# Optimization experiments

Measured on AMD Instinct MI355X. Metric: run time of the kernel, lower is better.

Reference implementation:

```python
import jax, jax.numpy as jnp
import numpy as np

B, T, S, D = 32, 1024, 1024, 512
VOCAB = 1000
INSERT_TOK = jnp.array([1, 2], dtype=jnp.int64)


def setup_inputs() -> dict:
    key = jax.random.key(0)
    k1, k2, k3, k4, k5 = jax.random.split(key, 5)
    input_var = jax.random.randint(k1, (B, T), 0, VOCAB, dtype=jnp.int64)
    output = jax.random.normal(k2, (B, T, D), jnp.float32)
    context = jax.random.normal(k3, (B, S, D), jnp.float32)
    # nn.Linear(2*dim, dim): weight [D, 2D], bias [D]
    W = jax.random.normal(k4, (D, 2 * D), jnp.float32) / np.sqrt(2 * D)
    b = jax.random.normal(k5, (D,), jnp.float32) * 0.01
    return {"input_var": input_var, "output": output, "context": context,
            "di": 0, "W": W, "b": b}


def _hard_align(input_var, src_len):
    """Replicates the python double-loop: sequential 'inserted' counter per batch.
    Returns (j, valid): j[b,i] = column of the 1.0 in attn row i (torch negative
    indices wrapped), valid[b,i] = whether row i gets any 1.0 at all."""
    bsz, tgt_len = input_var.shape
    flags = jnp.isin(input_var, INSERT_TOK)  # [B,T] is token an insert token

    def step(inserted, xi):
        i, flag = xi  # i: scalar position, flag: [B]
        cond = (src_len >= i - inserted)                    # gate, per batch
        ins2 = inserted + jnp.where(cond & flag, 1, 0)      # increment before write
        j = i - ins2 - 1
        j = jnp.where(j < 0, j + src_len, j)                # torch negative-index wrap
        return ins2, (j, cond)

    idxs = jnp.arange(1, tgt_len, dtype=jnp.int32)
    init = jnp.zeros((bsz,), jnp.int32)  # init_inserted()
    _, (j_rows, valid) = jax.lax.scan(step, init, (idxs, flags[:, 1:].T))
    j_rows = j_rows.T      # [B,T-1]
    valid = valid.T        # [B,T-1]
    # row 0: attn[b,0,0] = 1.0 always
    j_full = jnp.concatenate([jnp.zeros((bsz, 1), j_rows.dtype), j_rows], axis=1)
    valid_full = jnp.concatenate([jnp.ones((bsz, 1), bool), valid], axis=1)
    return j_full, valid_full


def reference(input_var, output, context, di, W, b):
    bsz, tgt_len, hid = output.shape
    src_len = context.shape[1]
    j, valid = _hard_align(input_var, src_len)              # [B,T], [B,T]
    vf = valid[:, :, None].astype(output.dtype)
    # hard one-hot attention matrix (as the module materializes it)
    attn = jax.nn.one_hot(j, src_len, dtype=output.dtype) * vf  # [B,T,S]
    # mix = bmm(attn, context) == masked gather of context rows
    mix = jnp.take_along_axis(context, j[:, :, None].astype(jnp.int32), axis=1) * vf
    combined = jnp.concatenate([mix, output], axis=-1)      # [B,T,2D]
    out = jnp.tanh(combined @ W.T + b)                      # [B,T,D]
    return out, attn
```

## Files before the change

### kernel.cpp

```cpp
#include <hip/hip_runtime.h>
#include <hip/hip_bf16.h>

#define B_ 32
#define T_ 1024
#define S_ 1024
#define D_ 512
#define M_ (B_*T_)
#define N_ D_
#define K_ (2*D_)

typedef __attribute__((ext_vector_type(8))) short bf16x8;
typedef __attribute__((ext_vector_type(4))) float f32x4;

__device__ inline unsigned short f2bf(float x) {
    union { float f; unsigned u; } v; v.f = x;
    unsigned r = v.u + 0x7FFFu + ((v.u >> 16) & 1u);
    return (unsigned short)(r >> 16);
}

__device__ inline float fast_tanh(float x) {
#if __has_builtin(__builtin_amdgcn_exp2f) && __has_builtin(__builtin_amdgcn_rcpf)
    const float e = __builtin_amdgcn_exp2f(x * 2.885390082f);
    const float r = __builtin_amdgcn_rcpf(e + 1.0f);
    return 1.0f - 2.0f * r;
#else
    return tanhf(x);
#endif
}

__global__ void align_kernel(const int* __restrict__ iv, int* __restrict__ jbuf) {
    const int b = blockIdx.x;
    const int lane = threadIdx.x;
    const int* row = iv + b * T_;
    int f[16];
    int local = 0;
    const int t0 = lane * 16;
    #pragma unroll
    for (int q = 0; q < 16; ++q) {
        const int t = t0 + q;
        const int tok = row[t];
        const int fl = (t > 0 && (tok == 1 || tok == 2)) ? 1 : 0;
        f[q] = fl;
        local += fl;
    }
    int incl = local;
    #pragma unroll
    for (int off = 1; off < 64; off <<= 1) {
        const int up = __shfl_up(incl, off, 64);
        if (lane >= off) incl += up;
    }
    int run = incl - local;
    #pragma unroll
    for (int q = 0; q < 16; ++q) {
        const int t = t0 + q;
        run += f[q];
        int j;
        if (t == 0) {
            j = 0;
        } else {
            j = t - run - 1;
            if (j < 0) j += S_;
        }
        jbuf[b * T_ + t] = j;
    }
}

__global__ void pack_w(const float* __restrict__ W, unsigned short* __restrict__ Wbf) {
    const int idx = blockIdx.x * blockDim.x + threadIdx.x;
    const f32x4 a = ((const f32x4*)W)[idx * 2];
    const f32x4 c = ((const f32x4*)W)[idx * 2 + 1];
    union { bf16x8 v; unsigned short u[8]; } pk;
    pk.u[0] = f2bf(a[0]); pk.u[1] = f2bf(a[1]); pk.u[2] = f2bf(a[2]); pk.u[3] = f2bf(a[3]);
    pk.u[4] = f2bf(c[0]); pk.u[5] = f2bf(c[1]); pk.u[6] = f2bf(c[2]); pk.u[7] = f2bf(c[3]);
    *(bf16x8*)(Wbf + (size_t)idx * 8) = pk.v;
}

__global__ __launch_bounds__(256)
void pack_a_attn(const float* __restrict__ ctx, const float* __restrict__ outp,
                 const int* __restrict__ jbuf, unsigned short* __restrict__ Abf,
                 float* __restrict__ attn) {
    const int m0 = blockIdx.x * 2;
    const int tid = threadIdx.x;
    const int r  = tid >> 7;
    const int kc = tid & 127;
    const int m  = m0 + r;
    const int k0 = kc * 8;
    const int j0 = jbuf[m0];
    const int j1 = jbuf[m0 + 1];

    const int jm = r ? j1 : j0;
    const float* src;
    if (k0 < D_) {
        const int b = m >> 10;
        src = ctx + ((size_t)(b * S_ + jm)) * D_ + k0;
    } else {
        src = outp + (size_t)m * D_ + (k0 - D_);
    }
    const f32x4 a = ((const f32x4*)src)[0];
    const f32x4 c = ((const f32x4*)src)[1];
    union { bf16x8 v; unsigned short u[8]; } pk;
    pk.u[0] = f2bf(a[0]); pk.u[1] = f2bf(a[1]); pk.u[2] = f2bf(a[2]); pk.u[3] = f2bf(a[3]);
    pk.u[4] = f2bf(c[0]); pk.u[5] = f2bf(c[1]); pk.u[6] = f2bf(c[2]); pk.u[7] = f2bf(c[3]);
    *(bf16x8*)(Abf + (size_t)m * K_ + k0) = pk.v;

    f32x4 v0 = {0.f, 0.f, 0.f, 0.f};
    f32x4 v1 = {0.f, 0.f, 0.f, 0.f};
    if ((j0 >> 2) == tid) v0[j0 & 3] = 1.0f;
    if ((j1 >> 2) == tid) v1[j1 & 3] = 1.0f;
    ((f32x4*)(attn + (size_t)m0 * S_))[tid] = v0;
    ((f32x4*)(attn + (size_t)(m0 + 1) * S_))[tid] = v1;
}

#define BM 128
#define BN 128
#define BK 64

template <bool PACKED>
__global__ __launch_bounds__(256)
void gemm_bt_tanh(const unsigned short* __restrict__ Abf,
                  const unsigned short* __restrict__ Wbf,
                  const float* __restrict__ bias,
                  float* __restrict__ out,
                  const float* __restrict__ ctx,
                  const float* __restrict__ outp,
                  const int* __restrict__ jbuf) {
    __shared__ unsigned short As[BM * BK];
    __shared__ unsigned short Bs[BN * BK];

    const int tid  = threadIdx.x;
    const int lane = tid & 63;
    const int wave = tid >> 6;
    const int wm = wave >> 1, wn = wave & 1;
    const int l16 = lane & 15, quad = lane >> 4;

    const int bm = blockIdx.x & 255;
    const int bn = blockIdx.x >> 8;
    const int mBase = bm * BM;
    const int nBase = bn * BN;

    f32x4 acc[4][4] = {};

    for (int ko = 0; ko < K_; ko += BK) {
        #pragma unroll
        for (int it = 0; it < 4; ++it) {
            const int chunk = it * 256 + tid;
            const int row = chunk >> 3;
            const int kc  = chunk & 7;
            const int gk8 = (kc ^ (row & 7)) * 8;
            if (PACKED) {
                const unsigned short* gA = Abf + (size_t)(mBase + row) * K_ + ko + gk8;
                __builtin_amdgcn_global_load_lds(
                    (const __attribute__((address_space(1))) void*)gA,
                    (__attribute__((address_space(3))) void*)(As + chunk * 8), 16, 0, 0);
            } else {
                const int kg = ko + gk8;
                const int m = mBase + row;
                const float* src;
                if (kg < D_) {
                    const int b = m >> 10;
                    src = ctx + ((size_t)(b * S_ + jbuf[m])) * D_ + kg;
                } else {
                    src = outp + (size_t)m * D_ + (kg - D_);
                }
                const f32x4 a = ((const f32x4*)src)[0];
                const f32x4 c = ((const f32x4*)src)[1];
                union { bf16x8 v; unsigned short u[8]; } pk;
                pk.u[0]=f2bf(a[0]); pk.u[1]=f2bf(a[1]); pk.u[2]=f2bf(a[2]); pk.u[3]=f2bf(a[3]);
                pk.u[4]=f2bf(c[0]); pk.u[5]=f2bf(c[1]); pk.u[6]=f2bf(c[2]); pk.u[7]=f2bf(c[3]);
                *(bf16x8*)(As + chunk * 8) = pk.v;
            }
        }
        #pragma unroll
        for (int it = 0; it < 4; ++it) {
            const int chunk = it * 256 + tid;
            const int row = chunk >> 3;
            const int kc  = chunk & 7;
            const int gk8 = (kc ^ (row & 7)) * 8;
            const unsigned short* gB = Wbf + (size_t)(nBase + row) * K_ + ko + gk8;
            __builtin_amdgcn_global_load_lds(
                (const __attribute__((address_space(1))) void*)gB,
                (__attribute__((address_space(3))) void*)(Bs + chunk * 8), 16, 0, 0);
        }
        __syncthreads();

        #pragma unroll
        for (int ks = 0; ks < 2; ++ks) {
            bf16x8 af[4], bfr[4];
            #pragma unroll
            for (int mt = 0; mt < 4; ++mt) {
                const int r = wm * 64 + mt * 16 + l16;
                const int q = ks * 4 + quad;
                af[mt] = *(const bf16x8*)&As[(r * 8 + (q ^ (r & 7))) * 8];
            }
            #pragma unroll
            for (int nt = 0; nt < 4; ++nt) {
                const int r = wn * 64 + nt * 16 + l16;
                const int q = ks * 4 + quad;
                bfr[nt] = *(const bf16x8*)&Bs[(r * 8 + (q ^ (r & 7))) * 8];
            }
            #pragma unroll
            for (int mt = 0; mt < 4; ++mt)
                #pragma unroll
                for (int nt = 0; nt < 4; ++nt)
                    acc[mt][nt] = __builtin_amdgcn_mfma_f32_16x16x32_bf16(
                        af[mt], bfr[nt], acc[mt][nt], 0, 0, 0);
        }
        __syncthreads();
    }

    #pragma unroll
    for (int nt = 0; nt < 4; ++nt) {
        const int n = nBase + wn * 64 + nt * 16 + l16;
        const float bv = bias[n];
        #pragma unroll
        for (int mt = 0; mt < 4; ++mt) {
            #pragma unroll
            for (int r = 0; r < 4; ++r) {
                const int m = mBase + wm * 64 + mt * 16 + quad * 4 + r;
                out[(size_t)m * N_ + n] = fast_tanh(acc[mt][nt][r] + bv);
            }
        }
    }
}

extern "C" void kernel_launch(void* const* d_in, const int* in_sizes, int n_in,
                              void* d_out, int out_size, void* d_ws, size_t ws_size,
                              hipStream_t stream) {
    const int*   iv   = (const int*)d_in[0];
    const float* outp = (const float*)d_in[1];
    const float* ctx  = (const float*)d_in[2];
    const float* W    = (const float*)d_in[4];
    const float* bias = (const float*)d_in[5];

    float* out  = (float*)d_out;
    float* attn = out + (size_t)M_ * N_;

    int* jbuf = (int*)d_ws;
    unsigned short* Wbf = (unsigned short*)((char*)d_ws + (size_t)M_ * 4);
    unsigned short* Abf = (unsigned short*)((char*)d_ws + (size_t)M_ * 4 + (size_t)N_ * K_ * 2);
    const size_t need_full = (size_t)M_ * 4 + (size_t)N_ * K_ * 2 + (size_t)M_ * K_ * 2;

    align_kernel<<<B_, 64, 0, stream>>>(iv, jbuf);
    pack_w<<<(N_ * K_ / 8) / 256, 256, 0, stream>>>(W, Wbf);

    if (ws_size >= need_full) {
        pack_a_attn<<<M_ / 2, 256, 0, stream>>>(ctx, outp, jbuf, Abf, attn);
        gemm_bt_tanh<true><<<(M_ / BM) * (N_ / BN), 256, 0, stream>>>(
            Abf, Wbf, bias, out, ctx, outp, jbuf);
    } else {
        pack_a_attn<<<M_ / 2, 256, 0, stream>>>(ctx, outp, jbuf, Abf, attn);
        gemm_bt_tanh<false><<<(M_ / BM) * (N_ / BN), 256, 0, stream>>>(
            Abf, Wbf, bias, out, ctx, outp, jbuf);
    }
}
```

Measured before the change: 379.8 us.

## Fuse A-packing and attn one-hot writes into the GEMM kernel

Drops the separate pack_a_attn pass that wrote a bf16 copy of the gathered context and output rows. The GEMM now loads fp32 rows directly, gathered through jbuf, converts them to bf16 with a packed conversion intrinsic, and stores them into swizzled LDS. Extra blocks in the same grid write the one-hot attn matrix, so that traffic can overlap with the GEMM. This removes a full write and re-read of the bf16 A buffer, at the cost of reading fp32 A four times, once per N tile, and losing the async global-to-LDS path for A.

```diff
diff --git a/kernel.cpp b/kernel.cpp
--- a/kernel.cpp
+++ b/kernel.cpp
@@ -16,6 +16,17 @@
     union { float f; unsigned u; } v; v.f = x;
     unsigned r = v.u + 0x7FFFu + ((v.u >> 16) & 1u);
     return (unsigned short)(r >> 16);
+}
+
+__device__ inline unsigned cvt2bf(float lo, float hi) {
+#if __has_builtin(__builtin_amdgcn_cvt_pk_bf16_f32)
+    typedef __attribute__((ext_vector_type(2))) __bf16 bf2;
+    union { bf2 v; unsigned u; } r;
+    r.v = __builtin_amdgcn_cvt_pk_bf16_f32(lo, hi);
+    return r.u;
+#else
+    return (unsigned)f2bf(lo) | ((unsigned)f2bf(hi) << 16);
+#endif
 }
 
 __device__ inline float fast_tanh(float x) {
@@ -69,105 +80,79 @@
     const int idx = blockIdx.x * blockDim.x + threadIdx.x;
     const f32x4 a = ((const f32x4*)W)[idx * 2];
     const f32x4 c = ((const f32x4*)W)[idx * 2 + 1];
-    union { bf16x8 v; unsigned short u[8]; } pk;
-    pk.u[0] = f2bf(a[0]); pk.u[1] = f2bf(a[1]); pk.u[2] = f2bf(a[2]); pk.u[3] = f2bf(a[3]);
-    pk.u[4] = f2bf(c[0]); pk.u[5] = f2bf(c[1]); pk.u[6] = f2bf(c[2]); pk.u[7] = f2bf(c[3]);
+    union { bf16x8 v; unsigned u[4]; } pk;
+    pk.u[0] = cvt2bf(a[0], a[1]); pk.u[1] = cvt2bf(a[2], a[3]);
+    pk.u[2] = cvt2bf(c[0], c[1]); pk.u[3] = cvt2bf(c[2], c[3]);
     *(bf16x8*)(Wbf + (size_t)idx * 8) = pk.v;
-}
-
-__global__ __launch_bounds__(256)
-void pack_a_attn(const float* __restrict__ ctx, const float* __restrict__ outp,
-                 const int* __restrict__ jbuf, unsigned short* __restrict__ Abf,
-                 float* __restrict__ attn) {
-    const int m0 = blockIdx.x * 2;
-    const int tid = threadIdx.x;
-    const int r  = tid >> 7;
-    const int kc = tid & 127;
-    const int m  = m0 + r;
-    const int k0 = kc * 8;
-    const int j0 = jbuf[m0];
-    const int j1 = jbuf[m0 + 1];
-
-    const int jm = r ? j1 : j0;
-    const float* src;
-    if (k0 < D_) {
-        const int b = m >> 10;
-        src = ctx + ((size_t)(b * S_ + jm)) * D_ + k0;
-    } else {
-        src = outp + (size_t)m * D_ + (k0 - D_);
-    }
-    const f32x4 a = ((const f32x4*)src)[0];
-    const f32x4 c = ((const f32x4*)src)[1];
-    union { bf16x8 v; unsigned short u[8]; } pk;
-    pk.u[0] = f2bf(a[0]); pk.u[1] = f2bf(a[1]); pk.u[2] = f2bf(a[2]); pk.u[3] = f2bf(a[3]);
-    pk.u[4] = f2bf(c[0]); pk.u[5] = f2bf(c[1]); pk.u[6] = f2bf(c[2]); pk.u[7] = f2bf(c[3]);
-    *(bf16x8*)(Abf + (size_t)m * K_ + k0) = pk.v;
-
-    f32x4 v0 = {0.f, 0.f, 0.f, 0.f};
-    f32x4 v1 = {0.f, 0.f, 0.f, 0.f};
-    if ((j0 >> 2) == tid) v0[j0 & 3] = 1.0f;
-    if ((j1 >> 2) == tid) v1[j1 & 3] = 1.0f;
-    ((f32x4*)(attn + (size_t)m0 * S_))[tid] = v0;
-    ((f32x4*)(attn + (size_t)(m0 + 1) * S_))[tid] = v1;
 }
 
 #define BM 128
 #define BN 128
 #define BK 64
-
-template <bool PACKED>
+#define NGEMM ((M_ / BM) * (N_ / BN))
+#define NATTN 512
+
 __global__ __launch_bounds__(256)
-void gemm_bt_tanh(const unsigned short* __restrict__ Abf,
-                  const unsigned short* __restrict__ Wbf,
-                  const float* __restrict__ bias,
-                  float* __restrict__ out,
-                  const float* __restrict__ ctx,
-                  const float* __restrict__ outp,
-                  const int* __restrict__ jbuf) {
+void gemm_attn(const unsigned short* __restrict__ Wbf,
+               const float* __restrict__ bias,
+               float* __restrict__ out,
+               float* __restrict__ attn,
+               const float* __restrict__ ctx,
+               const float* __restrict__ outp,
+               const int* __restrict__ jbuf) {
+    const int bx = blockIdx.x;
+    const int tid = threadIdx.x;
+
+    if (bx >= NGEMM) {
+        const int m0 = (bx - NGEMM) * 64;
+        #pragma unroll 4
+        for (int r = 0; r < 64; ++r) {
+            const int row = m0 + r;
+            const int j = jbuf[row];
+            f32x4 v = {0.f, 0.f, 0.f, 0.f};
+            if ((j >> 2) == tid) v[j & 3] = 1.0f;
+            ((f32x4*)(attn + (size_t)row * S_))[tid] = v;
+        }
+        return;
+    }
+
     __shared__ unsigned short As[BM * BK];
     __shared__ unsigned short Bs[BN * BK];
 
-    const int tid  = threadIdx.x;
     const int lane = tid & 63;
     const int wave = tid >> 6;
     const int wm = wave >> 1, wn = wave & 1;
     const int l16 = lane & 15, quad = lane >> 4;
 
-    const int bm = blockIdx.x & 255;
-    const int bn = blockIdx.x >> 8;
+    const int bm = bx & 255;
+    const int bn = bx >> 8;
     const int mBase = bm * BM;
     const int nBase = bn * BN;
 
+    const int arow = tid >> 1;
+    const int aseg = tid & 1;
+    const int am   = mBase + arow;
+    const int jm   = jbuf[am];
+    const float* actx = ctx + ((size_t)((am >> 10) * S_ + jm)) * D_ + aseg * 32;
+    const float* aoutp = outp + (size_t)am * D_ - D_ + aseg * 32;
+
     f32x4 acc[4][4] = {};
 
     for (int ko = 0; ko < K_; ko += BK) {
-        #pragma unroll
-        for (int it = 0; it < 4; ++it) {
-            const int chunk = it * 256 + tid;
-            const int row = chunk >> 3;
-            const int kc  = chunk & 7;
-            const int gk8 = (kc ^ (row & 7)) * 8;
-            if (PACKED) {
-                const unsigned short* gA = Abf + (size_t)(mBase + row) * K_ + ko + gk8;
-                __builtin_amdgcn_global_load_lds(
-                    (const __attribute__((address_space(1))) void*)gA,
-                    (__attribute__((address_space(3))) void*)(As + chunk * 8), 16, 0, 0);
-            } else {
-                const int kg = ko + gk8;
-                const int m = mBase + row;
-                const float* src;
-                if (kg < D_) {
-                    const int b = m >> 10;
-                    src = ctx + ((size_t)(b * S_ + jbuf[m])) * D_ + kg;
-                } else {
-                    src = outp + (size_t)m * D_ + (kg - D_);
-                }
-                const f32x4 a = ((const f32x4*)src)[0];
-                const f32x4 c = ((const f32x4*)src)[1];
-                union { bf16x8 v; unsigned short u[8]; } pk;
-                pk.u[0]=f2bf(a[0]); pk.u[1]=f2bf(a[1]); pk.u[2]=f2bf(a[2]); pk.u[3]=f2bf(a[3]);
-                pk.u[4]=f2bf(c[0]); pk.u[5]=f2bf(c[1]); pk.u[6]=f2bf(c[2]); pk.u[7]=f2bf(c[3]);
-                *(bf16x8*)(As + chunk * 8) = pk.v;
+        {
+            const float* srcA = (ko < D_) ? (actx + ko) : (aoutp + ko);
+            f32x4 fa[8];
+            #pragma unroll
+            for (int i = 0; i < 8; ++i) fa[i] = ((const f32x4*)srcA)[i];
+            #pragma unroll
+            for (int c = 0; c < 4; ++c) {
+                union { bf16x8 v; unsigned u[4]; } pk;
+                pk.u[0] = cvt2bf(fa[c*2][0],   fa[c*2][1]);
+                pk.u[1] = cvt2bf(fa[c*2][2],   fa[c*2][3]);
+                pk.u[2] = cvt2bf(fa[c*2+1][0], fa[c*2+1][1]);
+                pk.u[3] = cvt2bf(fa[c*2+1][2], fa[c*2+1][3]);
+                const int q = aseg * 4 + c;
+                *(bf16x8*)&As[(arow * 8 + (q ^ (arow & 7))) * 8] = pk.v;
             }
         }
         #pragma unroll
@@ -237,19 +222,8 @@
 
     int* jbuf = (int*)d_ws;
     unsigned short* Wbf = (unsigned short*)((char*)d_ws + (size_t)M_ * 4);
-    unsigned short* Abf = (unsigned short*)((char*)d_ws + (size_t)M_ * 4 + (size_t)N_ * K_ * 2);
-    const size_t need_full = (size_t)M_ * 4 + (size_t)N_ * K_ * 2 + (size_t)M_ * K_ * 2;
 
     align_kernel<<<B_, 64, 0, stream>>>(iv, jbuf);
     pack_w<<<(N_ * K_ / 8) / 256, 256, 0, stream>>>(W, Wbf);
-
-    if (ws_size >= need_full) {
-        pack_a_attn<<<M_ / 2, 256, 0, stream>>>(ctx, outp, jbuf, Abf, attn);
-        gemm_bt_tanh<true><<<(M_ / BM) * (N_ / BN), 256, 0, stream>>>(
-            Abf, Wbf, bias, out, ctx, outp, jbuf);
-    } else {
-        pack_a_attn<<<M_ / 2, 256, 0, stream>>>(ctx, outp, jbuf, Abf, attn);
-        gemm_bt_tanh<false><<<(M_ / BM) * (N_ / BN), 256, 0, stream>>>(
-            Abf, Wbf, bias, out, ctx, outp, jbuf);
-    }
-}
+    gemm_attn<<<NGEMM + NATTN, 256, 0, stream>>>(Wbf, bias, out, attn, ctx, outp, jbuf);
+}
```

Measured after the change: 364.5 us. -4.0%, faster.
